# Performance work log

Hardware: AMD Instinct MI355X
Metric: run time of the kernel (lower is better)

Reference implementation:

```python
import jax, jax.numpy as jnp
import numpy as np

LEVEL = 20            # module default -> 21 max-pool passes, kernels 1x1 .. 41x41 (H,W only)
K_SIG = 10.0          # init arg k: sigmoid weight sharpness
N_POOL = LEVEL + 1    # len(max_pool)
DENOM = N_POOL + 1    # torch: level = len(max_pool) + 1 = 22


def _edge3d(mask):
    # Equivalent to F.conv3d(mask, filt, padding=1) > 0 where filt is the
    # in-plane Laplacian: center 1, 4 H/W-neighbors -0.25, zeros elsewhere.
    p = jnp.pad(mask, ((0, 0), (0, 0), (0, 0), (1, 1), (1, 1)))
    lap = mask - 0.25 * (p[..., :-2, 1:-1] + p[..., 2:, 1:-1]
                         + p[..., 1:-1, :-2] + p[..., 1:-1, 2:])
    return (lap > 0).astype(jnp.float32)


def _mp3(x):
    # stride-1 3x3 max pool over H,W with same padding (pads with -inf like torch MaxPool)
    return jax.lax.reduce_window(x, -jnp.inf, jax.lax.max,
                                 (1, 1, 1, 3, 3), (1, 1, 1, 1, 1),
                                 ((0, 0), (0, 0), (0, 0), (1, 1), (1, 1)))


def _cal_dist(mask):
    edge = _edge3d(mask)  # [B,1,D,H,W] binary
    # maxpool with window (2k+1)x(2k+1) on a binary map == k cascaded 3x3 dilations,
    # so sum_{k=0}^{LEVEL} maxpool_{2k+1}(edge) is computed incrementally.
    def body(i, carry):
        e, acc = carry
        return (_mp3(e), acc + e)
    _, acc = jax.lax.fori_loop(0, N_POOL, body, (edge, jnp.zeros_like(edge)))
    return (DENOM - acc) / DENOM


def setup_inputs() -> dict:
    key = jax.random.key(0)
    k1, k2 = jax.random.split(key)
    outputs = jax.random.uniform(k1, (2, 1, 64, 256, 256), dtype=jnp.float32)
    masks = jax.random.randint(k2, (2, 1, 64, 256, 256), 0, 2, dtype=jnp.int32)
    return {"outputs": outputs, "masks": masks}


def reference(outputs, masks):
    eps = 1e-6
    m = masks.astype(jnp.float32)
    dist = _cal_dist(m)
    weight = jax.lax.stop_gradient(2.0 / (1.0 + jnp.exp(K_SIG * dist)))
    b = outputs.shape[0]
    ow = (outputs.astype(jnp.float32) * weight).reshape(b, -1)
    mw = (m * weight).reshape(b, -1)
    intersect = jnp.sum(ow * m.reshape(b, -1), axis=1)
    input_area = jnp.sum(ow, axis=1)
    target_area = jnp.sum(mw, axis=1)
    batch_loss = 1.0 - 2.0 * intersect / (input_area + target_area + 2.0 * eps)
    batch_loss = jnp.where(target_area == 0, 0.0, batch_loss)
    return batch_loss.mean()
```

## Files before the change

### kernel.cpp

```cpp
#include <hip/hip_runtime.h>
#include <stdint.h>

typedef unsigned long long u64;
typedef unsigned int u32;

__global__ __launch_bounds__(256) void bbsd_fused(const float* __restrict__ outputs,
                                                  const int* __restrict__ masks,
                                                  float* __restrict__ acc,
                                                  u32* __restrict__ cnt,
                                                  float* __restrict__ out) {
    __shared__ u64 rows[256][5];
    __shared__ u64 tmp[256][5];
    __shared__ float wtab[22];
    __shared__ float red[4][3];

    const int t = threadIdx.x;
    const int lane = t & 63, wv = t >> 6;
    const int slice = blockIdx.x & 127;
    const int h = blockIdx.x >> 7;
    const int b = slice >> 6;

    if (t < 22) wtab[t] = 2.0f / (1.0f + __expf(10.0f * (float)(t + 1) * (1.0f / 22.0f)));

    u64 m[4] = {0ull, 0ull, 0ull, 0ull};
    {
        const int4* mp = (const int4*)(masks + (size_t)slice * 65536 + (size_t)t * 256);
        #pragma unroll
        for (int g = 0; g < 64; ++g) {
            int4 v = mp[g];
            u64 nib = (u64)(v.x != 0) | ((u64)(v.y != 0) << 1)
                    | ((u64)(v.z != 0) << 2) | ((u64)(v.w != 0) << 3);
            m[g >> 4] |= nib << ((g & 15) * 4);
        }
        #pragma unroll
        for (int j = 0; j < 4; ++j) rows[t][j] = m[j];
    }
    __syncthreads();

    u64 c[4];
    {
        u64 up[4], dn[4];
        #pragma unroll
        for (int j = 0; j < 4; ++j) {
            up[j] = (t > 0)   ? rows[t - 1][j] : 0ull;
            dn[j] = (t < 255) ? rows[t + 1][j] : 0ull;
        }
        #pragma unroll
        for (int j = 0; j < 4; ++j) {
            u64 lf = (m[j] << 1) | (j > 0 ? (m[j - 1] >> 63) : 0ull);
            u64 rt = (m[j] >> 1) | (j < 3 ? (m[j + 1] << 63) : 0ull);
            c[j] = m[j] & ~(up[j] & dn[j] & lf & rt);
        }
    }

    u64 p[5][4];
    #pragma unroll
    for (int pl = 0; pl < 5; ++pl)
        #pragma unroll
        for (int j = 0; j < 4; ++j) p[pl][j] = 0ull;

    for (int k = 1; k <= 20; ++k) {
        u64 hh[4];
        #pragma unroll
        for (int j = 0; j < 4; ++j) {
            u64 lf = (c[j] << 1) | (j > 0 ? (c[j - 1] >> 63) : 0ull);
            u64 rt = (c[j] >> 1) | (j < 3 ? (c[j + 1] << 63) : 0ull);
            hh[j] = c[j] | lf | rt;
            tmp[t][j] = hh[j];
        }
        __syncthreads();
        #pragma unroll
        for (int j = 0; j < 4; ++j) {
            u64 u_ = (t > 0)   ? tmp[t - 1][j] : 0ull;
            u64 d_ = (t < 255) ? tmp[t + 1][j] : 0ull;
            u64 n = hh[j] | u_ | d_;
            u64 nw = n & ~c[j];
            c[j] = n;
            #pragma unroll
            for (int pl = 0; pl < 5; ++pl) {
                u64 sel = (u64)0 - (u64)((k >> pl) & 1);
                p[pl][j] |= nw & sel;
            }
        }
        int done = ((c[0] & c[1] & c[2] & c[3]) == 0xFFFFFFFFFFFFFFFFull) ? 1 : 0;
        if (__syncthreads_and(done)) break;
    }

    #pragma unroll
    for (int j = 0; j < 4; ++j) {
        u64 u_ = ~c[j];
        p[0][j] |= u_; p[2][j] |= u_; p[4][j] |= u_;
    }

    float s0 = 0.0f, s1 = 0.0f, s2 = 0.0f;
    {
        const float4* op4 = (const float4*)(outputs + (size_t)slice * 65536
                                            + (size_t)t * 256 + h * 128);
        #pragma unroll
        for (int i = 0; i < 32; ++i) {
            float4 o4 = op4[i];
            const int w = 2 * h + (i >> 4);
            const int sh = (i & 15) * 4;
            u32 P0 = (u32)(p[0][w] >> sh), P1 = (u32)(p[1][w] >> sh);
            u32 P2 = (u32)(p[2][w] >> sh), P3 = (u32)(p[3][w] >> sh);
            u32 P4 = (u32)(p[4][w] >> sh), M  = (u32)(m[w] >> sh);
            float ov[4] = {o4.x, o4.y, o4.z, o4.w};
            #pragma unroll
            for (int q = 0; q < 4; ++q) {
                int d0 = (int)((P0 >> q) & 1u)
                       | ((int)((P1 >> q) & 1u) << 1)
                       | ((int)((P2 >> q) & 1u) << 2)
                       | ((int)((P3 >> q) & 1u) << 3)
                       | ((int)((P4 >> q) & 1u) << 4);
                float wgt = wtab[d0];
                float wm = ((M >> q) & 1u) ? wgt : 0.0f;
                s0 += ov[q] * wgt;
                s1 += wm;
                s2 += ov[q] * wm;
            }
        }
    }

    #pragma unroll
    for (int off = 32; off > 0; off >>= 1) {
        s0 += __shfl_down(s0, off);
        s1 += __shfl_down(s1, off);
        s2 += __shfl_down(s2, off);
    }
    if (lane == 0) { red[wv][0] = s0; red[wv][1] = s1; red[wv][2] = s2; }
    __syncthreads();
    if (t < 3) {
        float v = red[0][t] + red[1][t] + red[2][t] + red[3][t];
        atomicAdd(&acc[b * 3 + t], v);
        __threadfence();
    }
    __syncthreads();

    if (t == 0) {
        u32 old = __hip_atomic_fetch_add(cnt, 1u, __ATOMIC_ACQ_REL, __HIP_MEMORY_SCOPE_AGENT);
        if (old == 255u) {
            float s[6];
            #pragma unroll
            for (int k = 0; k < 6; ++k)
                s[k] = __hip_atomic_load(&acc[k], __ATOMIC_ACQUIRE, __HIP_MEMORY_SCOPE_AGENT);
            float loss = 0.0f;
            #pragma unroll
            for (int bb = 0; bb < 2; ++bb) {
                float A = s[bb * 3 + 0], T = s[bb * 3 + 1], I = s[bb * 3 + 2];
                loss += (T == 0.0f) ? 0.0f : (1.0f - 2.0f * I / (A + T + 2e-6f));
            }
            out[0] = 0.5f * loss;
        }
    }
}

extern "C" void kernel_launch(void* const* d_in, const int* in_sizes, int n_in,
                              void* d_out, int out_size, void* d_ws, size_t ws_size,
                              hipStream_t stream) {
    const float* outputs = (const float*)d_in[0];
    const int* masks = (const int*)d_in[1];
    float* out = (float*)d_out;
    float* acc = (float*)d_ws;
    u32* cnt = (u32*)((char*)d_ws + 24);

    hipMemsetAsync(d_ws, 0, 32, stream);
    bbsd_fused<<<256, 256, 0, stream>>>(outputs, masks, acc, cnt, out);
}
```

Before: 120.9 us.

## Split each slice into row bands with halo to double block count

Each slice is now processed by four blocks, each owning 64 rows plus a 21-row halo on each side. This raises the grid from 256 to 512 blocks so more of the GPU's compute units are busy. Mask loading is restructured so consecutive threads read consecutive int4s and pack bits with 16-lane shuffles, giving coalesced reads. Per-pixel bit planes go through shared memory so the outputs read is also coalesced. The cost is that halo rows of the mask are loaded and dilated redundantly, plus the extra shared-memory staging.

Measured after the change: 129.0 us. 1.07x slower.

```diff
diff --git a/kernel.cpp b/kernel.cpp
--- a/kernel.cpp
+++ b/kernel.cpp
@@ -4,46 +4,68 @@
 typedef unsigned long long u64;
 typedef unsigned int u32;
 
-__global__ __launch_bounds__(256) void bbsd_fused(const float* __restrict__ outputs,
-                                                  const int* __restrict__ masks,
-                                                  float* __restrict__ acc,
-                                                  u32* __restrict__ cnt,
-                                                  float* __restrict__ out) {
-    __shared__ u64 rows[256][5];
-    __shared__ u64 tmp[256][5];
+#define HALO 21
+#define BAND 64
+#define MAXR (BAND + 2 * HALO)
+
+__global__ __launch_bounds__(256) void bbsd_band(const float* __restrict__ outputs,
+                                                 const int* __restrict__ masks,
+                                                 float* __restrict__ acc,
+                                                 u32* __restrict__ cnt,
+                                                 float* __restrict__ out) {
+    __shared__ u64 rows[MAXR][5];
+    __shared__ u64 tmp[MAXR][5];
+    __shared__ u64 pw[BAND][4][6];
     __shared__ float wtab[22];
     __shared__ float red[4][3];
 
     const int t = threadIdx.x;
     const int lane = t & 63, wv = t >> 6;
-    const int slice = blockIdx.x & 127;
-    const int h = blockIdx.x >> 7;
+    const int slice = blockIdx.x >> 2;
+    const int band = blockIdx.x & 3;
     const int b = slice >> 6;
+    const int r0 = band * BAND;
+    const int rs = (r0 - HALO < 0) ? 0 : r0 - HALO;
+    const int re = (r0 + BAND + HALO > 256) ? 256 : r0 + BAND + HALO;
+    const int R = re - rs;
+    const int ioff = r0 - rs;
 
     if (t < 22) wtab[t] = 2.0f / (1.0f + __expf(10.0f * (float)(t + 1) * (1.0f / 22.0f)));
 
-    u64 m[4] = {0ull, 0ull, 0ull, 0ull};
     {
-        const int4* mp = (const int4*)(masks + (size_t)slice * 65536 + (size_t)t * 256);
-        #pragma unroll
-        for (int g = 0; g < 64; ++g) {
-            int4 v = mp[g];
-            u64 nib = (u64)(v.x != 0) | ((u64)(v.y != 0) << 1)
-                    | ((u64)(v.z != 0) << 2) | ((u64)(v.w != 0) << 3);
-            m[g >> 4] |= nib << ((g & 15) * 4);
+        const int4* mp = (const int4*)(masks + (size_t)slice * 65536 + (size_t)rs * 256);
+        const int total = R * 64;
+        for (int idx = t; idx < total; idx += 256) {
+            int4 v = mp[idx];
+            u64 w = (u64)(v.x != 0) | ((u64)(v.y != 0) << 1)
+                  | ((u64)(v.z != 0) << 2) | ((u64)(v.w != 0) << 3);
+            w <<= (t & 15) * 4;
+            w |= __shfl_down(w, 8, 16);
+            w |= __shfl_down(w, 4, 16);
+            w |= __shfl_down(w, 2, 16);
+            w |= __shfl_down(w, 1, 16);
+            if ((t & 15) == 0) {
+                int widx = idx >> 4;
+                rows[widx >> 2][widx & 3] = w;
+            }
         }
-        #pragma unroll
-        for (int j = 0; j < 4; ++j) rows[t][j] = m[j];
     }
     __syncthreads();
 
-    u64 c[4];
-    {
+    u64 m[4] = {0, 0, 0, 0}, c[4] = {0, 0, 0, 0};
+    u64 p[5][4];
+    #pragma unroll
+    for (int pl = 0; pl < 5; ++pl)
+        #pragma unroll
+        for (int j = 0; j < 4; ++j) p[pl][j] = 0ull;
+
+    if (t < R) {
         u64 up[4], dn[4];
         #pragma unroll
         for (int j = 0; j < 4; ++j) {
-            up[j] = (t > 0)   ? rows[t - 1][j] : 0ull;
-            dn[j] = (t < 255) ? rows[t + 1][j] : 0ull;
+            m[j] = rows[t][j];
+            up[j] = (t > 0)     ? rows[t - 1][j] : 0ull;
+            dn[j] = (t < R - 1) ? rows[t + 1][j] : 0ull;
         }
         #pragma unroll
         for (int j = 0; j < 4; ++j) {
@@ -53,67 +75,74 @@
         }
     }
 
-    u64 p[5][4];
-    #pragma unroll
-    for (int pl = 0; pl < 5; ++pl)
-        #pragma unroll
-        for (int j = 0; j < 4; ++j) p[pl][j] = 0ull;
-
     for (int k = 1; k <= 20; ++k) {
-        u64 hh[4];
-        #pragma unroll
-        for (int j = 0; j < 4; ++j) {
-            u64 lf = (c[j] << 1) | (j > 0 ? (c[j - 1] >> 63) : 0ull);
-            u64 rt = (c[j] >> 1) | (j < 3 ? (c[j + 1] << 63) : 0ull);
-            hh[j] = c[j] | lf | rt;
-            tmp[t][j] = hh[j];
+        if (t < R) {
+            #pragma unroll
+            for (int j = 0; j < 4; ++j) {
+                u64 lf = (c[j] << 1) | (j > 0 ? (c[j - 1] >> 63) : 0ull);
+                u64 rt = (c[j] >> 1) | (j < 3 ? (c[j + 1] << 63) : 0ull);
+                tmp[t][j] = c[j] | lf | rt;
+            }
         }
         __syncthreads();
-        #pragma unroll
-        for (int j = 0; j < 4; ++j) {
-            u64 u_ = (t > 0)   ? tmp[t - 1][j] : 0ull;
-            u64 d_ = (t < 255) ? tmp[t + 1][j] : 0ull;
-            u64 n = hh[j] | u_ | d_;
-            u64 nw = n & ~c[j];
-            c[j] = n;
+        int done = 1;
+        if (t < R) {
             #pragma unroll
-            for (int pl = 0; pl < 5; ++pl) {
-                u64 sel = (u64)0 - (u64)((k >> pl) & 1);
-                p[pl][j] |= nw & sel;
+            for (int j = 0; j < 4; ++j) {
+                u64 u_ = (t > 0)     ? tmp[t - 1][j] : 0ull;
+                u64 d_ = (t < R - 1) ? tmp[t + 1][j] : 0ull;
+                u64 n = tmp[t][j] | u_ | d_;
+                u64 nw = n & ~c[j];
+                c[j] = n;
+                #pragma unroll
+                for (int pl = 0; pl < 5; ++pl) {
+                    u64 sel = (u64)0 - (u64)((k >> pl) & 1);
+                    p[pl][j] |= nw & sel;
+                }
             }
+            done = ((c[0] & c[1] & c[2] & c[3]) == 0xFFFFFFFFFFFFFFFFull) ? 1 : 0;
         }
-        int done = ((c[0] & c[1] & c[2] & c[3]) == 0xFFFFFFFFFFFFFFFFull) ? 1 : 0;
         if (__syncthreads_and(done)) break;
     }
 
-    #pragma unroll
-    for (int j = 0; j < 4; ++j) {
-        u64 u_ = ~c[j];
-        p[0][j] |= u_; p[2][j] |= u_; p[4][j] |= u_;
+    if (t >= ioff && t < ioff + BAND) {
+        const int i = t - ioff;
+        #pragma unroll
+        for (int j = 0; j < 4; ++j) {
+            u64 u_ = ~c[j];
+            pw[i][j][0] = p[0][j] | u_;
+            pw[i][j][1] = p[1][j];
+            pw[i][j][2] = p[2][j] | u_;
+            pw[i][j][3] = p[3][j];
+            pw[i][j][4] = p[4][j] | u_;
+            pw[i][j][5] = m[j];
+        }
     }
+    __syncthreads();
 
     float s0 = 0.0f, s1 = 0.0f, s2 = 0.0f;
     {
-        const float4* op4 = (const float4*)(outputs + (size_t)slice * 65536
-                                            + (size_t)t * 256 + h * 128);
+        const float4* op4 = (const float4*)outputs + (size_t)slice * 16384 + (size_t)r0 * 64;
         #pragma unroll
-        for (int i = 0; i < 32; ++i) {
-            float4 o4 = op4[i];
-            const int w = 2 * h + (i >> 4);
-            const int sh = (i & 15) * 4;
-            u32 P0 = (u32)(p[0][w] >> sh), P1 = (u32)(p[1][w] >> sh);
-            u32 P2 = (u32)(p[2][w] >> sh), P3 = (u32)(p[3][w] >> sh);
-            u32 P4 = (u32)(p[4][w] >> sh), M  = (u32)(m[w] >> sh);
+        for (int it = 0; it < 16; ++it) {
+            int idx = it * 256 + t;
+            float4 o4 = op4[idx];
+            int rl = idx >> 6;
+            int col = (idx * 4) & 255;
+            int w = col >> 6, sh = col & 63;
+            u64 P0 = pw[rl][w][0], P1 = pw[rl][w][1], P2 = pw[rl][w][2];
+            u64 P3 = pw[rl][w][3], P4 = pw[rl][w][4], M = pw[rl][w][5];
             float ov[4] = {o4.x, o4.y, o4.z, o4.w};
             #pragma unroll
             for (int q = 0; q < 4; ++q) {
-                int d0 = (int)((P0 >> q) & 1u)
-                       | ((int)((P1 >> q) & 1u) << 1)
-                       | ((int)((P2 >> q) & 1u) << 2)
-                       | ((int)((P3 >> q) & 1u) << 3)
-                       | ((int)((P4 >> q) & 1u) << 4);
+                int sq = sh + q;
+                int d0 = (int)((P0 >> sq) & 1ull)
+                       | ((int)((P1 >> sq) & 1ull) << 1)
+                       | ((int)((P2 >> sq) & 1ull) << 2)
+                       | ((int)((P3 >> sq) & 1ull) << 3)
+                       | ((int)((P4 >> sq) & 1ull) << 4);
                 float wgt = wtab[d0];
-                float wm = ((M >> q) & 1u) ? wgt : 0.0f;
+                float wm = ((M >> sq) & 1ull) ? wgt : 0.0f;
                 s0 += ov[q] * wgt;
                 s1 += wm;
                 s2 += ov[q] * wm;
@@ -138,7 +167,7 @@
 
     if (t == 0) {
         u32 old = __hip_atomic_fetch_add(cnt, 1u, __ATOMIC_ACQ_REL, __HIP_MEMORY_SCOPE_AGENT);
-        if (old == 255u) {
+        if (old == 511u) {
             float s[6];
             #pragma unroll
             for (int k = 0; k < 6; ++k)
@@ -164,5 +193,5 @@
     u32* cnt = (u32*)((char*)d_ws + 24);
 
     hipMemsetAsync(d_ws, 0, 32, stream);
-    bbsd_fused<<<256, 256, 0, stream>>>(outputs, masks, acc, cnt, out);
+    bbsd_band<<<512, 256, 0, stream>>>(outputs, masks, acc, cnt, out);
 }
```
